# Kernel tuning notes

Measured on AMD Instinct MI355X. Metric: run time of the kernel, lower is better.

The kernel has to match this reference:

```python
import jax, jax.numpy as jnp
import numpy as np

NUM_HEADS = 32
NUM_KV_HEADS = 8
HEAD_DIM = 128
HIDDEN = 4096
BASE = 10000.0


def setup_inputs() -> dict:
    key = jax.random.key(0)
    ks = jax.random.split(key, 9)
    bs, seq = 1, 2048
    x = jax.random.normal(ks[0], (bs, seq, HIDDEN), dtype=jnp.float32)
    position_ids = jnp.broadcast_to(jnp.arange(seq, dtype=jnp.int32), (bs, seq))
    s = 1.0 / np.sqrt(HIDDEN)
    wq = jax.random.normal(ks[1], (NUM_HEADS * HEAD_DIM, HIDDEN), dtype=jnp.float32) * s
    bq = jnp.zeros((NUM_HEADS * HEAD_DIM,), dtype=jnp.float32)
    wk = jax.random.normal(ks[2], (NUM_KV_HEADS * HEAD_DIM, HIDDEN), dtype=jnp.float32) * s
    bk = jnp.zeros((NUM_KV_HEADS * HEAD_DIM,), dtype=jnp.float32)
    wv = jax.random.normal(ks[3], (NUM_KV_HEADS * HEAD_DIM, HIDDEN), dtype=jnp.float32) * s
    bv = jnp.zeros((NUM_KV_HEADS * HEAD_DIM,), dtype=jnp.float32)
    wo = jax.random.normal(ks[4], (HIDDEN, NUM_HEADS * HEAD_DIM), dtype=jnp.float32) * s
    bo = jnp.zeros((HIDDEN,), dtype=jnp.float32)
    return {"x": x, "position_ids": position_ids, "wq": wq, "bq": bq,
            "wk": wk, "bk": bk, "wv": wv, "bv": bv, "wo": wo, "bo": bo}


def _rotate_half(t):
    h = t.shape[-1] // 2
    return jnp.concatenate([-t[..., h:], t[..., :h]], axis=-1)


def _rope_cos_sin(position_ids, dtype):
    # inv_freq: (head_dim/2,)
    inv_freq = 1.0 / (BASE ** (jnp.arange(0, HEAD_DIM, 2, dtype=jnp.float32) / HEAD_DIM))
    freqs = position_ids.astype(jnp.float32)[..., None] * inv_freq  # (bs, seq, hd/2)
    emb = jnp.concatenate([freqs, freqs], axis=-1)  # (bs, seq, hd)
    return jnp.cos(emb).astype(dtype), jnp.sin(emb).astype(dtype)


def reference(x, position_ids, wq, bq, wk, bk, wv, bv, wo, bo):
    bs, seq, _ = x.shape
    g = NUM_HEADS // NUM_KV_HEADS
    # projections -> (bs, heads, seq, head_dim)
    q = (x @ wq.T + bq).reshape(bs, seq, NUM_HEADS, HEAD_DIM).transpose(0, 2, 1, 3)
    k = (x @ wk.T + bk).reshape(bs, seq, NUM_KV_HEADS, HEAD_DIM).transpose(0, 2, 1, 3)
    v = (x @ wv.T + bv).reshape(bs, seq, NUM_KV_HEADS, HEAD_DIM).transpose(0, 2, 1, 3)
    cos, sin = _rope_cos_sin(position_ids, x.dtype)
    cos, sin = cos[:, None], sin[:, None]  # broadcast over heads
    q = q * cos + _rotate_half(q) * sin
    k = k * cos + _rotate_half(k) * sin
    # grouped attention without expanding kv (same math as repeat_kv)
    qg = q.reshape(bs, NUM_KV_HEADS, g, seq, HEAD_DIM)
    scores = jnp.einsum('bhgqd,bhkd->bhgqk', qg, k) / jnp.sqrt(
        jnp.asarray(HEAD_DIM, dtype=jnp.float32)).astype(x.dtype)
    probs = jax.nn.softmax(scores.astype(jnp.float32), axis=-1).astype(x.dtype)
    out = jnp.einsum('bhgqk,bhkd->bhgqd', probs, v)  # (bs, kvh, g, seq, hd)
    out = out.reshape(bs, NUM_HEADS, seq, HEAD_DIM).transpose(0, 2, 1, 3)
    out = out.reshape(bs, seq, NUM_HEADS * HEAD_DIM)
    return out @ wo.T + bo
```

## Files before the change

kernel.cpp:

```cpp
#include <hip/hip_runtime.h>
#include <stdint.h>

typedef unsigned short u16;
typedef unsigned long long u64;
typedef __attribute__((ext_vector_type(8))) short s8v;
typedef __attribute__((ext_vector_type(4))) float f4v;

#define MFMA(a, b, c) __builtin_amdgcn_mfma_f32_16x16x32_bf16((a), (b), (c), 0, 0, 0)

__device__ __forceinline__ u16 f2b(float f) {
  uint32_t x = __float_as_uint(f);
  x += 0x7fff + ((x >> 16) & 1);
  return (u16)(x >> 16);
}
__device__ __forceinline__ float b2f(u16 u) {
  return __uint_as_float(((uint32_t)u) << 16);
}

__device__ __forceinline__ void gll16(const void* g, void* l) {
  __builtin_amdgcn_global_load_lds((const __attribute__((address_space(1))) uint32_t*)g,
                                   (__attribute__((address_space(3))) uint32_t*)l, 16, 0, 0);
}
__device__ __forceinline__ void bar() { __builtin_amdgcn_s_barrier(); }

__global__ void cvt_all(const float* __restrict__ x, const float* __restrict__ wq,
                        const float* __restrict__ wk, const float* __restrict__ wv,
                        const float* __restrict__ wo,
                        u16* __restrict__ xb, u16* __restrict__ wqkv, u16* __restrict__ wob) {
  int i = blockIdx.x * 256 + threadIdx.x;
  const float* s; u16* d; size_t off;
  if      (i < 1048576) { s = x;  d = xb;   off = (size_t)i; }
  else if (i < 3145728) { s = wq; d = wqkv; off = (size_t)(i - 1048576); }
  else if (i < 3670016) { s = wk; d = wqkv + (size_t)16777216; off = (size_t)(i - 3145728); }
  else if (i < 4194304) { s = wv; d = wqkv + (size_t)20971520; off = (size_t)(i - 3670016); }
  else                  { s = wo; d = wob;  off = (size_t)(i - 4194304); }
  const float4* sp = (const float4*)(s + off * 8);
  float4 f0 = sp[0], f1 = sp[1];
  s8v o;
  o[0] = (short)f2b(f0.x); o[1] = (short)f2b(f0.y); o[2] = (short)f2b(f0.z); o[3] = (short)f2b(f0.w);
  o[4] = (short)f2b(f1.x); o[5] = (short)f2b(f1.y); o[6] = (short)f2b(f1.z); o[7] = (short)f2b(f1.w);
  *(s8v*)(d + off * 8) = o;
}

template <int BM, int MODE>
__global__ __launch_bounds__(512, 2) void gemm8p(
    const u16* __restrict__ A, const u16* __restrict__ Bact,
    const float* __restrict__ bias,
    float* __restrict__ Cf, u16* __restrict__ Cq, u16* __restrict__ Ck, u16* __restrict__ Cv,
    int K) {
  extern __shared__ u16 smem[];
  constexpr int AO = BM * 64;
  constexpr int BE = 2 * BM * 64;
  constexpr int BO = BE + 16384;
  constexpr int MI = BM / 64;
  constexpr int NH = BM / 64;

  const int tid = threadIdx.x;
  const int l = tid & 63, wv = tid >> 6;
  const int wm = wv >> 2, wn = wv & 3;
  const int lr = l & 15, lg = l >> 4;
  const int swz = 16 * (lr & 7);
  const int wrow = wm * (BM / 2);

  const int nwg = gridDim.x;
  int bid = blockIdx.x;
  bid = (bid & 7) * (nwg >> 3) + (bid >> 3);
  const int NB = 8;
  const int m0 = (bid / NB) * BM, n0 = (bid % NB) * 256;

  const size_t K64 = (size_t)64 * K;

  const int sr = tid >> 3;
  const int sc = ((tid & 7) ^ (sr & 7)) * 8;
  const u16* gA = A + (size_t)(m0 + sr) * K + sc;
  const u16* gB = Bact + (size_t)(n0 + sr) * K + sc;

  auto STA = [&](int P, int h, int kt) {
    gll16(gA + (size_t)(h * 64) * K + (size_t)kt * 64,
          smem + (P ? AO : 0) + h * 4096 + tid * 8);
  };
  auto STB = [&](int P, int h, int kt) {
    const u16* g = gB + (size_t)(h * 128) * K + (size_t)kt * 64;
    u16* d = smem + (P ? BO : BE) + h * 8192 + tid * 8;
    gll16(g, d);
    gll16(g + K64, d + 4096);
  };

  const char* smc = (const char*)smem;
  s8v a[MI][2], b0[2][2], b1[2][2];
  auto LDA = [&](int P, int QR) {
#pragma unroll
    for (int mi = 0; mi < MI; ++mi)
#pragma unroll
      for (int kk = 0; kk < 2; ++kk)
        a[mi][kk] = *(const s8v*)(smc + (P ? AO * 2 : 0) +
            (wrow + QR * (BM / 4) + mi * 16 + lr) * 128 + ((kk * 64 + lg * 16) ^ swz));
  };
  auto LDB = [&](int P, int QC, s8v bb[2][2]) {
#pragma unroll
    for (int ni = 0; ni < 2; ++ni)
#pragma unroll
      for (int kk = 0; kk < 2; ++kk)
        bb[ni][kk] = *(const s8v*)(smc + (P ? BO * 2 : BE * 2) +
            (wn * 64 + QC * 32 + ni * 16 + lr) * 128 + ((kk * 64 + lg * 16) ^ swz));
  };

  f4v acc[BM / 32][4];
#pragma unroll
  for (int i = 0; i < BM / 32; ++i)
#pragma unroll
    for (int j = 0; j < 4; ++j) acc[i][j] = {0.f, 0.f, 0.f, 0.f};

#define PHMF(QR, QC, B)                                                        \
  _Pragma("unroll") for (int mi = 0; mi < MI; ++mi)                            \
    _Pragma("unroll") for (int ni = 0; ni < 2; ++ni)                           \
      _Pragma("unroll") for (int kk = 0; kk < 2; ++kk)                         \
        acc[(QR) * MI + mi][(QC) * 2 + ni] =                                   \
            MFMA(a[mi][kk], B[ni][kk], acc[(QR) * MI + mi][(QC) * 2 + ni]);

  STB(0, 0, 0); STB(0, 1, 0);
#pragma unroll
  for (int h = 0; h < NH; ++h) STA(0, h, 0);
  STB(1, 0, 1); STB(1, 1, 1);
  asm volatile("s_waitcnt vmcnt(4)" ::: "memory");
  bar();

  const int ITERS = K >> 7;
  for (int i = 0; i < ITERS; ++i) {
    const int kn = 2 * i + 2;
    const bool more = (i + 1 < ITERS);
    LDA(0, 0); LDB(0, 0, b0); LDB(0, 1, b1);
    STA(1, 0, 2 * i + 1); STA(1, 1, 2 * i + 1);
    bar();
    __builtin_amdgcn_s_setprio(1);
    PHMF(0, 0, b0); PHMF(0, 1, b1);
    __builtin_amdgcn_s_setprio(0);
    bar();
    LDA(0, 1);
    if constexpr (NH > 2) STA(1, 2, 2 * i + 1);
    if (more) { STB(0, 0, kn); STB(0, 1, kn); }
    bar();
    __builtin_amdgcn_s_setprio(1);
    PHMF(1, 1, b1); PHMF(1, 0, b0);
    __builtin_amdgcn_s_setprio(0);
    if (more) asm volatile("s_waitcnt vmcnt(4)" ::: "memory");
    else      asm volatile("s_waitcnt vmcnt(0)" ::: "memory");
    bar();
    LDA(1, 0); LDB(1, 0, b0); LDB(1, 1, b1);
    if (more) { STA(0, 0, kn); STA(0, 1, kn); }
    bar();
    __builtin_amdgcn_s_setprio(1);
    PHMF(0, 0, b0); PHMF(0, 1, b1);
    __builtin_amdgcn_s_setprio(0);
    bar();
    LDA(1, 1);
    if (more) {
      if constexpr (NH > 2) STA(0, 2, kn);
      STB(1, 0, 2 * i + 3); STB(1, 1, 2 * i + 3);
    }
    bar();
    __builtin_amdgcn_s_setprio(1);
    PHMF(1, 1, b1); PHMF(1, 0, b0);
    __builtin_amdgcn_s_setprio(0);
    asm volatile("s_waitcnt vmcnt(4)" ::: "memory");
    bar();
  }
#undef PHMF

  bar();

  if constexpr (MODE == 2) {
#pragma unroll
    for (int fi = 0; fi < BM / 32; ++fi) {
      const int f0 = m0 + wrow + fi * 16;
      if (f0 >= 5120) {
#pragma unroll
        for (int fj = 0; fj < 4; ++fj)
#pragma unroll
          for (int r = 0; r < 4; ++r) {
            const int f = f0 + lg * 4 + r;
            const int tok = n0 + wn * 64 + fj * 16 + lr;
            Cv[(size_t)(f - 5120) * 2048 + tok] = f2b(acc[fi][fj][r] + bias[f]);
          }
      }
    }
    if (m0 + wrow < 5120) {
      u16* buf = smem + wv * 3328;
#pragma unroll
      for (int c = 0; c < 2; ++c) {
#pragma unroll
        for (int fj2 = 0; fj2 < 2; ++fj2) {
          const int fj = 2 * c + fj2;
          const int tl = fj2 * 16 + lr;
#pragma unroll
          for (int fi = 0; fi < BM / 32; ++fi) {
            const int f0 = m0 + wrow + fi * 16;
            if (f0 < 5120) {
#pragma unroll
              for (int r = 0; r < 4; ++r) {
                const int fl = fi * 16 + lg * 4 + r;
                buf[tl * 104 + fl] = f2b(acc[fi][fj][r] + bias[m0 + wrow + fl]);
              }
            }
          }
        }
        asm volatile("s_waitcnt lgkmcnt(0)" ::: "memory");
        const int row = l >> 1, half = l & 1;
        const int tok = n0 + wn * 64 + c * 32 + row;
#pragma unroll
        for (int i2 = 0; i2 < 6; ++i2) {
          const int flc = (2 * i2 + half) * 8;
          const int f = m0 + wrow + flc;
          if (f < 4096)
            *(s8v*)(Cq + (size_t)tok * 4096 + f) = *(const s8v*)(buf + row * 104 + flc);
          else if (f < 5120)
            *(s8v*)(Ck + (size_t)tok * 1024 + (f - 4096)) = *(const s8v*)(buf + row * 104 + flc);
        }
        asm volatile("s_waitcnt lgkmcnt(0)" ::: "memory");
        bar();
      }
    } else {
      bar(); bar();
    }
  } else {
    float* buf = (float*)smem + wv * 1088;
#pragma unroll
    for (int c = 0; c < 4; ++c) {
#pragma unroll
      for (int fi = 0; fi < BM / 32; ++fi)
#pragma unroll
        for (int r = 0; r < 4; ++r) {
          const int fl = fi * 16 + lg * 4 + r;
          buf[lr * 68 + fl] = acc[fi][c][r] + bias[m0 + wrow + fl];
        }
      asm volatile("s_waitcnt lgkmcnt(0)" ::: "memory");
      const int row = l >> 2, q4 = l & 3;
      const int tok = n0 + wn * 64 + c * 16 + row;
      float* g = Cf + (size_t)tok * 4096 + m0 + wrow + q4 * 16;
      const float* src = buf + row * 68 + q4 * 16;
#pragma unroll
      for (int i2 = 0; i2 < 4; ++i2)
        *(f4v*)(g + i2 * 4) = *(const f4v*)(src + i2 * 4);
      asm volatile("s_waitcnt lgkmcnt(0)" ::: "memory");
    }
  }
}

__global__ void rope_kernel(u16* __restrict__ q, u16* __restrict__ k, const int* __restrict__ pos) {
  int i = blockIdx.x * 256 + threadIdx.x;
  const int NQ = 2048 * 32 * 64;
  const int NK = 2048 * 8 * 64;
  u16* buf;
  int m, d, stride, h;
  if (i < NQ) { buf = q; m = i >> 11; h = (i >> 6) & 31; d = i & 63; stride = 4096; }
  else {
    i -= NQ; if (i >= NK) return;
    buf = k; m = i >> 9; h = (i >> 6) & 7; d = i & 63; stride = 1024;
  }
  size_t base = (size_t)m * stride + h * 128 + d;
  float a = b2f(buf[base]), b = b2f(buf[base + 64]);
  float p = (float)pos[m];
  float ang = p * exp2f(-0.20762050593045952f * (float)d);
  float s, c;
  sincosf(ang, &s, &c);
  buf[base]      = f2b(a * c - b * s);
  buf[base + 64] = f2b(b * c + a * s);
}

__global__ __launch_bounds__(512, 4) void attn_kernel(const u16* __restrict__ Q, const u16* __restrict__ Kb,
                                                      const u16* __restrict__ Vt, u16* __restrict__ Ao) {
  __shared__ __align__(16) u16 Ks[2][64 * 128];
  __shared__ __align__(16) u16 Vs[2][128 * 64];
  __shared__ __align__(16) u16 Ps[8][16 * 64];
  const int tid = threadIdx.x;
  const int l = tid & 63, wv = tid >> 6;
  const int lr = l & 15, lg = l >> 4;
  const int head = blockIdx.x >> 4, qt = blockIdx.x & 15;
  const int kh = head >> 2;
  const int qrow = qt * 128 + wv * 16 + lr;

  s8v qf[4];
#pragma unroll
  for (int s = 0; s < 4; ++s)
    qf[s] = *(const s8v*)&Q[(size_t)qrow * 4096 + head * 128 + s * 32 + lg * 8];

  f4v zero = {0.f, 0.f, 0.f, 0.f};
  f4v ao[8];
#pragma unroll
  for (int tt = 0; tt < 8; ++tt) ao[tt] = zero;
  float mrun = -1e30f, lrun = 0.f;

  const int ki0 = tid, ki1 = tid + 512;
  const int kr0 = ki0 >> 4, kc0 = (ki0 & 15) ^ (kr0 & 7);
  const int kr1 = ki1 >> 4, kc1 = (ki1 & 15) ^ (kr1 & 7);
  const int vr0 = ki0 >> 3, vc0 = (ki0 & 7) ^ (vr0 & 7);
  const int vr1 = ki1 >> 3, vc1 = (ki1 & 7) ^ (vr1 & 7);
  const u16* Kg = Kb + kh * 128;
  const u16* Vg = Vt + (size_t)(kh * 128) * 2048;
  const u16* kp0 = Kg + (size_t)kr0 * 1024 + kc0 * 8;
  const u16* kp1 = Kg + (size_t)kr1 * 1024 + kc1 * 8;
  const u16* vp0 = Vg + (size_t)vr0 * 2048 + vc0 * 8;
  const u16* vp1 = Vg + (size_t)vr1 * 2048 + vc1 * 8;

  auto stage = [&](int b, int t) {
    gll16(kp0 + (size_t)t * 1024, (char*)Ks[b] + ki0 * 16);
    gll16(kp1 + (size_t)t * 1024, (char*)Ks[b] + ki1 * 16);
    gll16(vp0 + t,                (char*)Vs[b] + ki0 * 16);
    gll16(vp1 + t,                (char*)Vs[b] + ki1 * 16);
  };

  char* PwB = (char*)Ps[wv];
  const int swz = 16 * (lr & 7);
  const float C2 = 0.12753102f;

  stage(0, 0);
  __syncthreads();

  for (int t = 0; t < 2048; t += 64) {
    const int cur = (t >> 6) & 1;
    if (t + 64 < 2048) stage(cur ^ 1, t + 64);
    const char* KsB = (const char*)Ks[cur];
    const char* VsB = (const char*)Vs[cur];

    f4v c[4];
#pragma unroll
    for (int j = 0; j < 4; ++j) c[j] = zero;
#pragma unroll
    for (int s = 0; s < 4; ++s) {
#pragma unroll
      for (int j = 0; j < 4; ++j) {
        s8v kf = *(const s8v*)(KsB + (16 * j + lr) * 256 + (((4 * s + lg) * 16) ^ swz));
        c[j] = MFMA(kf, qf[s], c[j]);
      }
    }

    float mx = fmaxf(fmaxf(c[0][0], c[0][1]), fmaxf(c[0][2], c[0][3]));
#pragma unroll
    for (int j = 1; j < 4; ++j)
      mx = fmaxf(mx, fmaxf(fmaxf(c[j][0], c[j][1]), fmaxf(c[j][2], c[j][3])));
    mx = fmaxf(mx, __shfl_xor(mx, 16));
    mx = fmaxf(mx, __shfl_xor(mx, 32));
    float m2x = mx * C2;

    if (!__all(m2x - mrun <= 8.f)) {
      float mnew = fmaxf(mrun, m2x);
      float alpha = __builtin_amdgcn_exp2f(mrun - mnew);
      float ar[4];
#pragma unroll
      for (int r = 0; r < 4; ++r) ar[r] = __shfl(alpha, 4 * lg + r);
#pragma unroll
      for (int tt = 0; tt < 8; ++tt)
#pragma unroll
        for (int r = 0; r < 4; ++r) ao[tt][r] *= ar[r];
      lrun *= alpha;
      mrun = mnew;
    }

    float rs = 0.f;
#pragma unroll
    for (int j = 0; j < 4; ++j) {
      float p0 = __builtin_amdgcn_exp2f(__builtin_fmaf(c[j][0], C2, -mrun));
      float p1 = __builtin_amdgcn_exp2f(__builtin_fmaf(c[j][1], C2, -mrun));
      float p2 = __builtin_amdgcn_exp2f(__builtin_fmaf(c[j][2], C2, -mrun));
      float p3 = __builtin_amdgcn_exp2f(__builtin_fmaf(c[j][3], C2, -mrun));
      rs += (p0 + p1) + (p2 + p3);
      uint32_t lo = (uint32_t)f2b(p0) | ((uint32_t)f2b(p1) << 16);
      uint32_t hi = (uint32_t)f2b(p2) | ((uint32_t)f2b(p3) << 16);
      u64 pak = (u64)lo | ((u64)hi << 32);
      *(u64*)(PwB + lr * 128 + ((32 * j + 8 * lg) ^ swz)) = pak;
    }
    rs += __shfl_xor(rs, 16);
    rs += __shfl_xor(rs, 32);
    lrun += rs;

#pragma unroll
    for (int h = 0; h < 2; ++h) {
      s8v pf = *(const s8v*)(PwB + lr * 128 + ((64 * h + 16 * lg) ^ swz));
#pragma unroll
      for (int tt = 0; tt < 8; ++tt) {
        s8v vf = *(const s8v*)(VsB + (16 * tt + lr) * 128 + (((4 * h + lg) * 16) ^ swz));
        ao[tt] = MFMA(pf, vf, ao[tt]);
      }
    }

    __syncthreads();
  }

  float inv = 1.f / lrun;
  float ir[4];
#pragma unroll
  for (int r = 0; r < 4; ++r) ir[r] = __shfl(inv, 4 * lg + r);
#pragma unroll
  for (int tt = 0; tt < 8; ++tt)
#pragma unroll
    for (int r = 0; r < 4; ++r)
      Ao[(size_t)(qt * 128 + wv * 16 + 4 * lg + r) * 4096 + head * 128 + 16 * tt + lr] =
          f2b(ao[tt][r] * ir[r]);
}

extern "C" void kernel_launch(void* const* d_in, const int* in_sizes, int n_in,
                              void* d_out, int out_size, void* d_ws, size_t ws_size,
                              hipStream_t stream) {
  const float* x  = (const float*)d_in[0];
  const int*   pos = (const int*)d_in[1];
  const float* wq = (const float*)d_in[2];
  const float* bq = (const float*)d_in[3];
  const float* wk = (const float*)d_in[4];
  const float* bk = (const float*)d_in[5];
  const float* wv = (const float*)d_in[6];
  const float* bv = (const float*)d_in[7];
  const float* wo = (const float*)d_in[8];
  const float* bo = (const float*)d_in[9];
  float* out = (float*)d_out;

  char* ws = (char*)d_ws;
  u16* xb   = (u16*)(ws + 0);
  u16* wqkv = (u16*)(ws + 16777216);
  u16* wob  = (u16*)(ws + 67108864);
  u16* qb   = (u16*)(ws + 100663296);
  u16* kb   = (u16*)(ws + 117440512);
  u16* vT   = (u16*)(ws + 121634816);
  u16* ab   = (u16*)(ws + 125829120);
  float* bqkv = (float*)(ws + 142606336);

  hipMemcpyAsync(bqkv,        bq, 4096 * sizeof(float), hipMemcpyDeviceToDevice, stream);
  hipMemcpyAsync(bqkv + 4096, bk, 1024 * sizeof(float), hipMemcpyDeviceToDevice, stream);
  hipMemcpyAsync(bqkv + 5120, bv, 1024 * sizeof(float), hipMemcpyDeviceToDevice, stream);

  cvt_all<<<24576, 256, 0, stream>>>(x, wq, wk, wv, wo, xb, wqkv, wob);

  gemm8p<192, 2><<<256, 512, 114688, stream>>>(wqkv, xb, bqkv,
                                               nullptr, qb, kb, vT, 4096);
  rope_kernel<<<(2048 * 32 * 64 + 2048 * 8 * 64) / 256, 256, 0, stream>>>(qb, kb, pos);
  attn_kernel<<<512, 512, 0, stream>>>(qb, kb, vT, ab);
  gemm8p<128, 0><<<256, 512, 98304, stream>>>(wob, ab, bo,
                                              out, nullptr, nullptr, nullptr, 4096);
}
```

Before: 327.5 us.

## Halve GEMM N-tile to 128 tokens, doubling workgroups and occupancy

Both projection GEMMs now use a 128-wide token tile instead of 256. This doubles the grid to 512 workgroups, cuts LDS and accumulator registers per block, and raises launch_bounds occupancy to 4. The aim is better CU fill and latency hiding on a 256-CU part, where 256 blocks gave only one wave of work. The cost is lower arithmetic intensity per block and more redundant weight-tile loads, and the B-load pipeline and epilogue were restructured to match.

```diff
diff --git a/kernel.cpp b/kernel.cpp
--- a/kernel.cpp
+++ b/kernel.cpp
@@ -43,7 +43,7 @@
 }
 
 template <int BM, int MODE>
-__global__ __launch_bounds__(512, 2) void gemm8p(
+__global__ __launch_bounds__(512, 4) void gemm4p(
     const u16* __restrict__ A, const u16* __restrict__ Bact,
     const float* __restrict__ bias,
     float* __restrict__ Cf, u16* __restrict__ Cq, u16* __restrict__ Ck, u16* __restrict__ Cv,
@@ -51,7 +51,7 @@
   extern __shared__ u16 smem[];
   constexpr int AO = BM * 64;
   constexpr int BE = 2 * BM * 64;
-  constexpr int BO = BE + 16384;
+  constexpr int BO = BE + 128 * 64;
   constexpr int MI = BM / 64;
   constexpr int NH = BM / 64;
 
@@ -65,8 +65,8 @@
   const int nwg = gridDim.x;
   int bid = blockIdx.x;
   bid = (bid & 7) * (nwg >> 3) + (bid >> 3);
-  const int NB = 8;
-  const int m0 = (bid / NB) * BM, n0 = (bid % NB) * 256;
+  const int NB = 16;
+  const int m0 = (bid / NB) * BM, n0 = (bid % NB) * 128;
 
   const size_t K64 = (size_t)64 * K;
 
@@ -79,9 +79,9 @@
     gll16(gA + (size_t)(h * 64) * K + (size_t)kt * 64,
           smem + (P ? AO : 0) + h * 4096 + tid * 8);
   };
-  auto STB = [&](int P, int h, int kt) {
-    const u16* g = gB + (size_t)(h * 128) * K + (size_t)kt * 64;
-    u16* d = smem + (P ? BO : BE) + h * 8192 + tid * 8;
+  auto STB = [&](int P, int kt) {
+    const u16* g = gB + (size_t)kt * 64;
+    u16* d = smem + (P ? BO : BE) + tid * 8;
     gll16(g, d);
     gll16(g + K64, d + 4096);
   };
@@ -96,73 +96,62 @@
         a[mi][kk] = *(const s8v*)(smc + (P ? AO * 2 : 0) +
             (wrow + QR * (BM / 4) + mi * 16 + lr) * 128 + ((kk * 64 + lg * 16) ^ swz));
   };
-  auto LDB = [&](int P, int QC, s8v bb[2][2]) {
+  auto LDB = [&](int P, s8v bb[2][2]) {
 #pragma unroll
     for (int ni = 0; ni < 2; ++ni)
 #pragma unroll
       for (int kk = 0; kk < 2; ++kk)
         bb[ni][kk] = *(const s8v*)(smc + (P ? BO * 2 : BE * 2) +
-            (wn * 64 + QC * 32 + ni * 16 + lr) * 128 + ((kk * 64 + lg * 16) ^ swz));
+            (wn * 32 + ni * 16 + lr) * 128 + ((kk * 64 + lg * 16) ^ swz));
   };
 
-  f4v acc[BM / 32][4];
-#pragma unroll
-  for (int i = 0; i < BM / 32; ++i)
-#pragma unroll
-    for (int j = 0; j < 4; ++j) acc[i][j] = {0.f, 0.f, 0.f, 0.f};
-
-#define PHMF(QR, QC, B)                                                        \
+  f4v acc[2 * MI][2];
+#pragma unroll
+  for (int i = 0; i < 2 * MI; ++i)
+#pragma unroll
+    for (int j = 0; j < 2; ++j) acc[i][j] = {0.f, 0.f, 0.f, 0.f};
+
+#define PHMF(QR, B)                                                            \
+  __builtin_amdgcn_s_setprio(1);                                               \
   _Pragma("unroll") for (int mi = 0; mi < MI; ++mi)                            \
     _Pragma("unroll") for (int ni = 0; ni < 2; ++ni)                           \
       _Pragma("unroll") for (int kk = 0; kk < 2; ++kk)                         \
-        acc[(QR) * MI + mi][(QC) * 2 + ni] =                                   \
-            MFMA(a[mi][kk], B[ni][kk], acc[(QR) * MI + mi][(QC) * 2 + ni]);
-
-  STB(0, 0, 0); STB(0, 1, 0);
+        acc[(QR) * MI + mi][ni] =                                              \
+            MFMA(a[mi][kk], B[ni][kk], acc[(QR) * MI + mi][ni]);               \
+  __builtin_amdgcn_s_setprio(0);
+
 #pragma unroll
   for (int h = 0; h < NH; ++h) STA(0, h, 0);
-  STB(1, 0, 1); STB(1, 1, 1);
-  asm volatile("s_waitcnt vmcnt(4)" ::: "memory");
+  STB(0, 0);
+  STB(1, 1);
+  asm volatile("s_waitcnt vmcnt(2)" ::: "memory");
   bar();
 
   const int ITERS = K >> 7;
   for (int i = 0; i < ITERS; ++i) {
     const int kn = 2 * i + 2;
     const bool more = (i + 1 < ITERS);
-    LDA(0, 0); LDB(0, 0, b0); LDB(0, 1, b1);
+    LDA(0, 0); LDB(0, b0);
     STA(1, 0, 2 * i + 1); STA(1, 1, 2 * i + 1);
-    bar();
-    __builtin_amdgcn_s_setprio(1);
-    PHMF(0, 0, b0); PHMF(0, 1, b1);
-    __builtin_amdgcn_s_setprio(0);
-    bar();
+    bar(); PHMF(0, b0); bar();
     LDA(0, 1);
     if constexpr (NH > 2) STA(1, 2, 2 * i + 1);
-    if (more) { STB(0, 0, kn); STB(0, 1, kn); }
-    bar();
-    __builtin_amdgcn_s_setprio(1);
-    PHMF(1, 1, b1); PHMF(1, 0, b0);
-    __builtin_amdgcn_s_setprio(0);
-    if (more) asm volatile("s_waitcnt vmcnt(4)" ::: "memory");
+    if (more) STB(0, kn);
+    bar(); PHMF(1, b0);
+    if (more) asm volatile("s_waitcnt vmcnt(2)" ::: "memory");
     else      asm volatile("s_waitcnt vmcnt(0)" ::: "memory");
     bar();
-    LDA(1, 0); LDB(1, 0, b0); LDB(1, 1, b1);
+    LDA(1, 0); LDB(1, b1);
     if (more) { STA(0, 0, kn); STA(0, 1, kn); }
-    bar();
-    __builtin_amdgcn_s_setprio(1);
-    PHMF(0, 0, b0); PHMF(0, 1, b1);
-    __builtin_amdgcn_s_setprio(0);
-    bar();
+    bar(); PHMF(0, b1); bar();
     LDA(1, 1);
     if (more) {
       if constexpr (NH > 2) STA(0, 2, kn);
-      STB(1, 0, 2 * i + 3); STB(1, 1, 2 * i + 3);
-    }
-    bar();
-    __builtin_amdgcn_s_setprio(1);
-    PHMF(1, 1, b1); PHMF(1, 0, b0);
-    __builtin_amdgcn_s_setprio(0);
-    asm volatile("s_waitcnt vmcnt(4)" ::: "memory");
+      STB(1, 2 * i + 3);
+    }
+    bar(); PHMF(1, b1);
+    if (more) asm volatile("s_waitcnt vmcnt(2)" ::: "memory");
+    else      asm volatile("s_waitcnt vmcnt(0)" ::: "memory");
     bar();
   }
 #undef PHMF
@@ -171,71 +160,64 @@
 
   if constexpr (MODE == 2) {
 #pragma unroll
-    for (int fi = 0; fi < BM / 32; ++fi) {
-      const int f0 = m0 + wrow + fi * 16;
+    for (int ai = 0; ai < 2 * MI; ++ai) {
+      const int f0 = m0 + wrow + ai * 16;
       if (f0 >= 5120) {
 #pragma unroll
-        for (int fj = 0; fj < 4; ++fj)
+        for (int ni = 0; ni < 2; ++ni)
 #pragma unroll
           for (int r = 0; r < 4; ++r) {
             const int f = f0 + lg * 4 + r;
-            const int tok = n0 + wn * 64 + fj * 16 + lr;
-            Cv[(size_t)(f - 5120) * 2048 + tok] = f2b(acc[fi][fj][r] + bias[f]);
+            const int tok = n0 + wn * 32 + ni * 16 + lr;
+            Cv[(size_t)(f - 5120) * 2048 + tok] = f2b(acc[ai][ni][r] + bias[f]);
           }
       }
     }
     if (m0 + wrow < 5120) {
       u16* buf = smem + wv * 3328;
 #pragma unroll
-      for (int c = 0; c < 2; ++c) {
-#pragma unroll
-        for (int fj2 = 0; fj2 < 2; ++fj2) {
-          const int fj = 2 * c + fj2;
-          const int tl = fj2 * 16 + lr;
-#pragma unroll
-          for (int fi = 0; fi < BM / 32; ++fi) {
-            const int f0 = m0 + wrow + fi * 16;
-            if (f0 < 5120) {
-#pragma unroll
-              for (int r = 0; r < 4; ++r) {
-                const int fl = fi * 16 + lg * 4 + r;
-                buf[tl * 104 + fl] = f2b(acc[fi][fj][r] + bias[m0 + wrow + fl]);
-              }
+      for (int ni = 0; ni < 2; ++ni) {
+        const int tl = ni * 16 + lr;
+#pragma unroll
+        for (int ai = 0; ai < 2 * MI; ++ai) {
+          const int f0 = m0 + wrow + ai * 16;
+          if (f0 < 5120) {
+#pragma unroll
+            for (int r = 0; r < 4; ++r) {
+              const int fl = ai * 16 + lg * 4 + r;
+              buf[tl * 104 + fl] = f2b(acc[ai][ni][r] + bias[m0 + wrow + fl]);
             }
           }
         }
-        asm volatile("s_waitcnt lgkmcnt(0)" ::: "memory");
-        const int row = l >> 1, half = l & 1;
-        const int tok = n0 + wn * 64 + c * 32 + row;
-#pragma unroll
-        for (int i2 = 0; i2 < 6; ++i2) {
-          const int flc = (2 * i2 + half) * 8;
-          const int f = m0 + wrow + flc;
-          if (f < 4096)
-            *(s8v*)(Cq + (size_t)tok * 4096 + f) = *(const s8v*)(buf + row * 104 + flc);
-          else if (f < 5120)
-            *(s8v*)(Ck + (size_t)tok * 1024 + (f - 4096)) = *(const s8v*)(buf + row * 104 + flc);
-        }
-        asm volatile("s_waitcnt lgkmcnt(0)" ::: "memory");
-        bar();
       }
-    } else {
-      bar(); bar();
+      asm volatile("s_waitcnt lgkmcnt(0)" ::: "memory");
+      const int row = l >> 1, half = l & 1;
+      const int tok = n0 + wn * 32 + row;
+#pragma unroll
+      for (int i2 = 0; i2 < 6; ++i2) {
+        const int flc = (2 * i2 + half) * 8;
+        const int f = m0 + wrow + flc;
+        if (f < 4096)
+          *(s8v*)(Cq + (size_t)tok * 4096 + f) = *(const s8v*)(buf + row * 104 + flc);
+        else if (f < 5120)
+          *(s8v*)(Ck + (size_t)tok * 1024 + (f - 4096)) = *(const s8v*)(buf + row * 104 + flc);
+      }
+      asm volatile("s_waitcnt lgkmcnt(0)" ::: "memory");
     }
   } else {
     float* buf = (float*)smem + wv * 1088;
 #pragma unroll
-    for (int c = 0; c < 4; ++c) {
-#pragma unroll
-      for (int fi = 0; fi < BM / 32; ++fi)
+    for (int c = 0; c < 2; ++c) {
+#pragma unroll
+      for (int ai = 0; ai < 2 * MI; ++ai)
 #pragma unroll
         for (int r = 0; r < 4; ++r) {
-          const int fl = fi * 16 + lg * 4 + r;
-          buf[lr * 68 + fl] = acc[fi][c][r] + bias[m0 + wrow + fl];
+          const int fl = ai * 16 + lg * 4 + r;
+          buf[lr * 68 + fl] = acc[ai][c][r] + bias[m0 + wrow + fl];
         }
       asm volatile("s_waitcnt lgkmcnt(0)" ::: "memory");
       const int row = l >> 2, q4 = l & 3;
-      const int tok = n0 + wn * 64 + c * 16 + row;
+      const int tok = n0 + wn * 32 + c * 16 + row;
       float* g = Cf + (size_t)tok * 4096 + m0 + wrow + q4 * 16;
       const float* src = buf + row * 68 + q4 * 16;
 #pragma unroll
@@ -429,10 +411,10 @@
 
   cvt_all<<<24576, 256, 0, stream>>>(x, wq, wk, wv, wo, xb, wqkv, wob);
 
-  gemm8p<192, 2><<<256, 512, 114688, stream>>>(wqkv, xb, bqkv,
-                                               nullptr, qb, kb, vT, 4096);
+  gemm4p<192, 2><<<512, 512, 81920, stream>>>(wqkv, xb, bqkv,
+                                              nullptr, qb, kb, vT, 4096);
   rope_kernel<<<(2048 * 32 * 64 + 2048 * 8 * 64) / 256, 256, 0, stream>>>(qb, kb, pos);
   attn_kernel<<<512, 512, 0, stream>>>(qb, kb, vT, ab);
-  gemm8p<128, 0><<<256, 512, 98304, stream>>>(wob, ab, bo,
+  gemm4p<128, 0><<<512, 512, 65536, stream>>>(wob, ab, bo,
                                               out, nullptr, nullptr, nullptr, 4096);
 }
```

New measurement: 406.9 us. 1.24x slower.

## Give each attention wave two query tiles and drop K/V double buffering

Applied to the files above, without the earlier changes.

The attention kernel now uses 256 threads per block, and each wave handles 32 query rows as two 16-row halves. Each K fragment read from LDS therefore feeds two MFMAs, and each V fragment likewise feeds two. The K/V tiles are single-buffered and loaded synchronously, with barriers before and after each load, which shrinks LDS use so more blocks can be resident. The cost is that global loads no longer overlap with compute inside a block, and register pressure rises from doubled accumulators and Q fragments, which may cut occupancy.

```diff
diff --git a/kernel.cpp b/kernel.cpp
--- a/kernel.cpp
+++ b/kernel.cpp
@@ -267,135 +267,144 @@
   buf[base + 64] = f2b(b * c + a * s);
 }
 
-__global__ __launch_bounds__(512, 4) void attn_kernel(const u16* __restrict__ Q, const u16* __restrict__ Kb,
+__global__ __launch_bounds__(256, 2) void attn_kernel(const u16* __restrict__ Q, const u16* __restrict__ Kb,
                                                       const u16* __restrict__ Vt, u16* __restrict__ Ao) {
-  __shared__ __align__(16) u16 Ks[2][64 * 128];
-  __shared__ __align__(16) u16 Vs[2][128 * 64];
-  __shared__ __align__(16) u16 Ps[8][16 * 64];
+  __shared__ __align__(16) u16 Ks[64 * 128];
+  __shared__ __align__(16) u16 Vs[128 * 64];
+  __shared__ __align__(16) u16 Ps[4][32 * 64];
   const int tid = threadIdx.x;
   const int l = tid & 63, wv = tid >> 6;
   const int lr = l & 15, lg = l >> 4;
   const int head = blockIdx.x >> 4, qt = blockIdx.x & 15;
   const int kh = head >> 2;
-  const int qrow = qt * 128 + wv * 16 + lr;
-
-  s8v qf[4];
-#pragma unroll
-  for (int s = 0; s < 4; ++s)
-    qf[s] = *(const s8v*)&Q[(size_t)qrow * 4096 + head * 128 + s * 32 + lg * 8];
+  const int qrow = qt * 128 + wv * 32 + lr;
+
+  s8v qf[2][4];
+#pragma unroll
+  for (int qh = 0; qh < 2; ++qh)
+#pragma unroll
+    for (int s = 0; s < 4; ++s)
+      qf[qh][s] = *(const s8v*)&Q[(size_t)(qrow + qh * 16) * 4096 + head * 128 + s * 32 + lg * 8];
 
   f4v zero = {0.f, 0.f, 0.f, 0.f};
-  f4v ao[8];
-#pragma unroll
-  for (int tt = 0; tt < 8; ++tt) ao[tt] = zero;
-  float mrun = -1e30f, lrun = 0.f;
-
-  const int ki0 = tid, ki1 = tid + 512;
-  const int kr0 = ki0 >> 4, kc0 = (ki0 & 15) ^ (kr0 & 7);
-  const int kr1 = ki1 >> 4, kc1 = (ki1 & 15) ^ (kr1 & 7);
-  const int vr0 = ki0 >> 3, vc0 = (ki0 & 7) ^ (vr0 & 7);
-  const int vr1 = ki1 >> 3, vc1 = (ki1 & 7) ^ (vr1 & 7);
+  f4v ao[2][8];
+#pragma unroll
+  for (int qh = 0; qh < 2; ++qh)
+#pragma unroll
+    for (int tt = 0; tt < 8; ++tt) ao[qh][tt] = zero;
+  float mrun[2] = {-1e30f, -1e30f}, lrun[2] = {0.f, 0.f};
+
   const u16* Kg = Kb + kh * 128;
   const u16* Vg = Vt + (size_t)(kh * 128) * 2048;
-  const u16* kp0 = Kg + (size_t)kr0 * 1024 + kc0 * 8;
-  const u16* kp1 = Kg + (size_t)kr1 * 1024 + kc1 * 8;
-  const u16* vp0 = Vg + (size_t)vr0 * 2048 + vc0 * 8;
-  const u16* vp1 = Vg + (size_t)vr1 * 2048 + vc1 * 8;
-
-  auto stage = [&](int b, int t) {
-    gll16(kp0 + (size_t)t * 1024, (char*)Ks[b] + ki0 * 16);
-    gll16(kp1 + (size_t)t * 1024, (char*)Ks[b] + ki1 * 16);
-    gll16(vp0 + t,                (char*)Vs[b] + ki0 * 16);
-    gll16(vp1 + t,                (char*)Vs[b] + ki1 * 16);
-  };
-
+  const u16* kp[4];
+  const u16* vp[4];
+#pragma unroll
+  for (int p = 0; p < 4; ++p) {
+    const int ki = tid + 256 * p;
+    const int kr = ki >> 4, kc = (ki & 15) ^ (kr & 7);
+    kp[p] = Kg + (size_t)kr * 1024 + kc * 8;
+    const int vr = ki >> 3, vc = (ki & 7) ^ (vr & 7);
+    vp[p] = Vg + (size_t)vr * 2048 + vc * 8;
+  }
+
+  char* KsB = (char*)Ks;
+  char* VsB = (char*)Vs;
   char* PwB = (char*)Ps[wv];
   const int swz = 16 * (lr & 7);
   const float C2 = 0.12753102f;
 
-  stage(0, 0);
-  __syncthreads();
-
   for (int t = 0; t < 2048; t += 64) {
-    const int cur = (t >> 6) & 1;
-    if (t + 64 < 2048) stage(cur ^ 1, t + 64);
-    const char* KsB = (const char*)Ks[cur];
-    const char* VsB = (const char*)Vs[cur];
-
-    f4v c[4];
-#pragma unroll
-    for (int j = 0; j < 4; ++j) c[j] = zero;
+    __syncthreads();
+#pragma unroll
+    for (int p = 0; p < 4; ++p) {
+      gll16(kp[p] + (size_t)t * 1024, KsB + (tid + 256 * p) * 16);
+      gll16(vp[p] + t,                VsB + (tid + 256 * p) * 16);
+    }
+    __syncthreads();
+
+    f4v c[2][4];
+#pragma unroll
+    for (int qh = 0; qh < 2; ++qh)
+#pragma unroll
+      for (int j = 0; j < 4; ++j) c[qh][j] = zero;
 #pragma unroll
     for (int s = 0; s < 4; ++s) {
 #pragma unroll
       for (int j = 0; j < 4; ++j) {
         s8v kf = *(const s8v*)(KsB + (16 * j + lr) * 256 + (((4 * s + lg) * 16) ^ swz));
-        c[j] = MFMA(kf, qf[s], c[j]);
-      }
-    }
-
-    float mx = fmaxf(fmaxf(c[0][0], c[0][1]), fmaxf(c[0][2], c[0][3]));
-#pragma unroll
-    for (int j = 1; j < 4; ++j)
-      mx = fmaxf(mx, fmaxf(fmaxf(c[j][0], c[j][1]), fmaxf(c[j][2], c[j][3])));
-    mx = fmaxf(mx, __shfl_xor(mx, 16));
-    mx = fmaxf(mx, __shfl_xor(mx, 32));
-    float m2x = mx * C2;
-
-    if (!__all(m2x - mrun <= 8.f)) {
-      float mnew = fmaxf(mrun, m2x);
-      float alpha = __builtin_amdgcn_exp2f(mrun - mnew);
-      float ar[4];
-#pragma unroll
-      for (int r = 0; r < 4; ++r) ar[r] = __shfl(alpha, 4 * lg + r);
-#pragma unroll
-      for (int tt = 0; tt < 8; ++tt)
-#pragma unroll
-        for (int r = 0; r < 4; ++r) ao[tt][r] *= ar[r];
-      lrun *= alpha;
-      mrun = mnew;
-    }
-
-    float rs = 0.f;
-#pragma unroll
-    for (int j = 0; j < 4; ++j) {
-      float p0 = __builtin_amdgcn_exp2f(__builtin_fmaf(c[j][0], C2, -mrun));
-      float p1 = __builtin_amdgcn_exp2f(__builtin_fmaf(c[j][1], C2, -mrun));
-      float p2 = __builtin_amdgcn_exp2f(__builtin_fmaf(c[j][2], C2, -mrun));
-      float p3 = __builtin_amdgcn_exp2f(__builtin_fmaf(c[j][3], C2, -mrun));
-      rs += (p0 + p1) + (p2 + p3);
-      uint32_t lo = (uint32_t)f2b(p0) | ((uint32_t)f2b(p1) << 16);
-      uint32_t hi = (uint32_t)f2b(p2) | ((uint32_t)f2b(p3) << 16);
-      u64 pak = (u64)lo | ((u64)hi << 32);
-      *(u64*)(PwB + lr * 128 + ((32 * j + 8 * lg) ^ swz)) = pak;
-    }
-    rs += __shfl_xor(rs, 16);
-    rs += __shfl_xor(rs, 32);
-    lrun += rs;
+        c[0][j] = MFMA(kf, qf[0][s], c[0][j]);
+        c[1][j] = MFMA(kf, qf[1][s], c[1][j]);
+      }
+    }
+
+#pragma unroll
+    for (int qh = 0; qh < 2; ++qh) {
+      float mx = fmaxf(fmaxf(c[qh][0][0], c[qh][0][1]), fmaxf(c[qh][0][2], c[qh][0][3]));
+#pragma unroll
+      for (int j = 1; j < 4; ++j)
+        mx = fmaxf(mx, fmaxf(fmaxf(c[qh][j][0], c[qh][j][1]), fmaxf(c[qh][j][2], c[qh][j][3])));
+      mx = fmaxf(mx, __shfl_xor(mx, 16));
+      mx = fmaxf(mx, __shfl_xor(mx, 32));
+      float m2x = mx * C2;
+
+      if (!__all(m2x - mrun[qh] <= 8.f)) {
+        float mnew = fmaxf(mrun[qh], m2x);
+        float alpha = __builtin_amdgcn_exp2f(mrun[qh] - mnew);
+        float ar[4];
+#pragma unroll
+        for (int r = 0; r < 4; ++r) ar[r] = __shfl(alpha, 4 * lg + r);
+#pragma unroll
+        for (int tt = 0; tt < 8; ++tt)
+#pragma unroll
+          for (int r = 0; r < 4; ++r) ao[qh][tt][r] *= ar[r];
+        lrun[qh] *= alpha;
+        mrun[qh] = mnew;
+      }
+
+      float rs = 0.f;
+#pragma unroll
+      for (int j = 0; j < 4; ++j) {
+        float p0 = __builtin_amdgcn_exp2f(__builtin_fmaf(c[qh][j][0], C2, -mrun[qh]));
+        float p1 = __builtin_amdgcn_exp2f(__builtin_fmaf(c[qh][j][1], C2, -mrun[qh]));
+        float p2 = __builtin_amdgcn_exp2f(__builtin_fmaf(c[qh][j][2], C2, -mrun[qh]));
+        float p3 = __builtin_amdgcn_exp2f(__builtin_fmaf(c[qh][j][3], C2, -mrun[qh]));
+        rs += (p0 + p1) + (p2 + p3);
+        uint32_t lo = (uint32_t)f2b(p0) | ((uint32_t)f2b(p1) << 16);
+        uint32_t hi = (uint32_t)f2b(p2) | ((uint32_t)f2b(p3) << 16);
+        u64 pak = (u64)lo | ((u64)hi << 32);
+        *(u64*)(PwB + (qh * 16 + lr) * 128 + ((32 * j + 8 * lg) ^ swz)) = pak;
+      }
+      rs += __shfl_xor(rs, 16);
+      rs += __shfl_xor(rs, 32);
+      lrun[qh] += rs;
+    }
 
 #pragma unroll
     for (int h = 0; h < 2; ++h) {
-      s8v pf = *(const s8v*)(PwB + lr * 128 + ((64 * h + 16 * lg) ^ swz));
+      s8v pf0 = *(const s8v*)(PwB + lr * 128 + ((64 * h + 16 * lg) ^ swz));
+      s8v pf1 = *(const s8v*)(PwB + (16 + lr) * 128 + ((64 * h + 16 * lg) ^ swz));
 #pragma unroll
       for (int tt = 0; tt < 8; ++tt) {
         s8v vf = *(const s8v*)(VsB + (16 * tt + lr) * 128 + (((4 * h + lg) * 16) ^ swz));
-        ao[tt] = MFMA(pf, vf, ao[tt]);
-      }
-    }
-
-    __syncthreads();
-  }
-
-  float inv = 1.f / lrun;
-  float ir[4];
-#pragma unroll
-  for (int r = 0; r < 4; ++r) ir[r] = __shfl(inv, 4 * lg + r);
-#pragma unroll
-  for (int tt = 0; tt < 8; ++tt)
-#pragma unroll
-    for (int r = 0; r < 4; ++r)
-      Ao[(size_t)(qt * 128 + wv * 16 + 4 * lg + r) * 4096 + head * 128 + 16 * tt + lr] =
-          f2b(ao[tt][r] * ir[r]);
+        ao[0][tt] = MFMA(pf0, vf, ao[0][tt]);
+        ao[1][tt] = MFMA(pf1, vf, ao[1][tt]);
+      }
+    }
+  }
+
+#pragma unroll
+  for (int qh = 0; qh < 2; ++qh) {
+    float inv = 1.f / lrun[qh];
+    float ir[4];
+#pragma unroll
+    for (int r = 0; r < 4; ++r) ir[r] = __shfl(inv, 4 * lg + r);
+#pragma unroll
+    for (int tt = 0; tt < 8; ++tt)
+#pragma unroll
+      for (int r = 0; r < 4; ++r)
+        Ao[(size_t)(qt * 128 + wv * 32 + qh * 16 + 4 * lg + r) * 4096 + head * 128 + 16 * tt + lr] =
+            f2b(ao[qh][tt][r] * ir[r]);
+  }
 }
 
 extern "C" void kernel_launch(void* const* d_in, const int* in_sizes, int n_in,
@@ -432,7 +441,7 @@
   gemm8p<192, 2><<<256, 512, 114688, stream>>>(wqkv, xb, bqkv,
                                                nullptr, qb, kb, vT, 4096);
   rope_kernel<<<(2048 * 32 * 64 + 2048 * 8 * 64) / 256, 256, 0, stream>>>(qb, kb, pos);
-  attn_kernel<<<512, 512, 0, stream>>>(qb, kb, vT, ab);
+  attn_kernel<<<512, 256, 0, stream>>>(qb, kb, vT, ab);
   gemm8p<128, 0><<<256, 512, 98304, stream>>>(wob, ab, bo,
                                               out, nullptr, nullptr, nullptr, 4096);
 }
```

Result: no change. 325.6 us (median of 2 runs) (-0.6%).
